# Kernel optimization log

Measured on AMD Instinct MI355X. Metric: run time of the kernel, lower is better.

Reference implementation:

```python
import jax, jax.numpy as jnp
import numpy as np

B, N, NFEAT, NHID, NOUT, NMLP, NCLASS = 32, 1024, 128, 64, 64, 128, 2
ALPHA = 0.2  # leaky relu slope
NEG = -9e15


def setup_inputs() -> dict:
    key = jax.random.key(0)
    ks = jax.random.split(key, 12)
    x = jax.random.normal(ks[0], (B, N, NFEAT), dtype=jnp.float32)
    x_mask = (jax.random.uniform(ks[1], (B, N)) < 0.9).astype(jnp.float32)
    adj = (jax.random.uniform(ks[2], (B, N, N)) < 0.05).astype(jnp.float32)
    adj = jnp.maximum(adj, jnp.eye(N, dtype=jnp.float32)[None])  # self loops
    s = 0.02
    W0 = jax.random.normal(ks[3], (NFEAT, NHID), dtype=jnp.float32) * s
    a0 = jax.random.normal(ks[4], (2 * NHID, 1), dtype=jnp.float32) * s
    Wout = jax.random.normal(ks[5], (NHID, NOUT), dtype=jnp.float32) * s
    aout = jax.random.normal(ks[6], (2 * NOUT, 1), dtype=jnp.float32) * s
    W1 = jax.random.normal(ks[7], (NOUT, NMLP), dtype=jnp.float32) * s
    b1 = jnp.zeros((NMLP,), dtype=jnp.float32)
    W2 = jax.random.normal(ks[8], (NMLP, NCLASS), dtype=jnp.float32) * s
    b2 = jnp.zeros((NCLASS,), dtype=jnp.float32)
    return {"x": x, "x_mask": x_mask, "adj": adj, "W0": W0, "a0": a0,
            "Wout": Wout, "aout": aout, "W1": W1, "b1": b1, "W2": W2, "b2": b2}


def _gat_layer(h, adj, W, a):
    # h: [B,N,F_in], W: [F_in,F_out], a: [2*F_out,1]
    Wh = jnp.einsum('bnf,fh->bnh', h, W)                 # [B,N,F_out]
    d = W.shape[1]
    f1 = Wh @ a[:d]                                      # [B,N,1]
    f2 = Wh @ a[d:]                                      # [B,N,1]
    e = jax.nn.leaky_relu(f1 + jnp.swapaxes(f2, 1, 2), ALPHA)  # [B,N,N]
    e = jnp.where(adj > 0, e, NEG)
    attn = jax.nn.softmax(e, axis=-1)
    return jnp.einsum('bnm,bmh->bnh', attn, Wh)


def reference(x, x_mask, adj, W0, a0, Wout, aout, W1, b1, W2, b2):
    # Only head 0 reaches out_att in the original (zip truncation); dropout is
    # identity in eval mode.
    h = jax.nn.elu(_gat_layer(x, adj, W0, a0))           # concat=True -> elu
    h = jax.nn.elu(_gat_layer(h, adj, Wout, aout))       # F.elu applied outside
    m = x_mask[..., None]
    g = jnp.sum(h * m, axis=1) / jnp.maximum(jnp.sum(x_mask, axis=1, keepdims=True), 1.0)  # masked mean readout [B,NOUT]
    return jax.nn.relu(g @ W1 + b1) @ W2 + b2            # [B,NCLASS]
```

## Files before the change

### kernel.cpp

```cpp
#include <hip/hip_runtime.h>
#include <math.h>

#define BB 32
#define NN 1024
#define NFEAT 128
#define ALPHA 0.2f
#define MAXD 128

#define WH1_TILE_BLOCKS (BB * NN / 64)
#define NBR_BLOCKS (BB * NN / 4)

template<int FIN>
__device__ __forceinline__ void wh_tile_body(
    const int blk, const int tid,
    const float* __restrict__ hin, const float* __restrict__ W,
    const float* __restrict__ a, float* __restrict__ Wh,
    float* __restrict__ f1, float* __restrict__ f2) {
  const int tx = tid & 15;
  const int ty = tid >> 4;
  const int row0 = blk * 64 + ty * 4;

  float4 acc[4];
#pragma unroll
  for (int i = 0; i < 4; ++i) acc[i] = make_float4(0.f, 0.f, 0.f, 0.f);

#pragma unroll 4
  for (int k = 0; k < FIN; k += 4) {
    float4 wv[4];
#pragma unroll
    for (int i = 0; i < 4; ++i)
      wv[i] = *reinterpret_cast<const float4*>(&W[(size_t)(k + i) * 64 + tx * 4]);
#pragma unroll
    for (int i = 0; i < 4; ++i) {
      const float4 xv = *reinterpret_cast<const float4*>(
          &hin[(size_t)(row0 + i) * FIN + k]);
      acc[i].x = fmaf(xv.x, wv[0].x, acc[i].x);
      acc[i].y = fmaf(xv.x, wv[0].y, acc[i].y);
      acc[i].z = fmaf(xv.x, wv[0].z, acc[i].z);
      acc[i].w = fmaf(xv.x, wv[0].w, acc[i].w);
      acc[i].x = fmaf(xv.y, wv[1].x, acc[i].x);
      acc[i].y = fmaf(xv.y, wv[1].y, acc[i].y);
      acc[i].z = fmaf(xv.y, wv[1].z, acc[i].z);
      acc[i].w = fmaf(xv.y, wv[1].w, acc[i].w);
      acc[i].x = fmaf(xv.z, wv[2].x, acc[i].x);
      acc[i].y = fmaf(xv.z, wv[2].y, acc[i].y);
      acc[i].z = fmaf(xv.z, wv[2].z, acc[i].z);
      acc[i].w = fmaf(xv.z, wv[2].w, acc[i].w);
      acc[i].x = fmaf(xv.w, wv[3].x, acc[i].x);
      acc[i].y = fmaf(xv.w, wv[3].y, acc[i].y);
      acc[i].z = fmaf(xv.w, wv[3].z, acc[i].z);
      acc[i].w = fmaf(xv.w, wv[3].w, acc[i].w);
    }
  }

  const float4 av1 = *reinterpret_cast<const float4*>(&a[tx * 4]);
  const float4 av2 = *reinterpret_cast<const float4*>(&a[64 + tx * 4]);
#pragma unroll
  for (int i = 0; i < 4; ++i) {
    const int row = row0 + i;
    *reinterpret_cast<float4*>(&Wh[(size_t)row * 64 + tx * 4]) = acc[i];
    float c1 = acc[i].x * av1.x + acc[i].y * av1.y + acc[i].z * av1.z + acc[i].w * av1.w;
    float c2 = acc[i].x * av2.x + acc[i].y * av2.y + acc[i].z * av2.z + acc[i].w * av2.w;
#pragma unroll
    for (int off = 8; off > 0; off >>= 1) {
      c1 += __shfl_xor(c1, off, 64);
      c2 += __shfl_xor(c2, off, 64);
    }
    if (tx == 0) { f1[row] = c1; f2[row] = c2; }
  }
}

__global__ __launch_bounds__(256) void wh1_nbr_kernel(
    const float* __restrict__ x, const float* __restrict__ W0,
    const float* __restrict__ a0, float* __restrict__ Wh,
    float* __restrict__ f1, float* __restrict__ f2,
    const float* __restrict__ adj, unsigned short* __restrict__ nbr,
    int* __restrict__ cnt) {
  if (blockIdx.x < WH1_TILE_BLOCKS) {
    wh_tile_body<NFEAT>(blockIdx.x, threadIdx.x, x, W0, a0, Wh, f1, f2);
    return;
  }
  const int row = (blockIdx.x - WH1_TILE_BLOCKS) * 4 + (threadIdx.x >> 6);
  const int lane = threadIdx.x & 63;
  const float* adjrow = adj + (size_t)row * NN;
  unsigned short* nrow = nbr + (size_t)row * MAXD;
  int count = 0;
#pragma unroll
  for (int c = 0; c < NN / 64; ++c) {
    const float av = adjrow[c * 64 + lane];
    const bool on = av > 0.f;
    const unsigned long long mask = __ballot(on);
    const int pos = __popcll(mask & ((1ull << lane) - 1ull));
    if (on && count + pos < MAXD)
      nrow[count + pos] = (unsigned short)(c * 64 + lane);
    count += __popcll(mask);
  }
  if (lane == 0) cnt[row] = count < MAXD ? count : MAXD;
}

template<bool FUSE>
__global__ __launch_bounds__(256) void attn_kernel(
    const unsigned short* __restrict__ nbr, const int* __restrict__ cnt,
    const float* __restrict__ f1, const float* __restrict__ f2,
    const float* __restrict__ Wh,
    const float* __restrict__ Wnext, const float* __restrict__ anext,
    float* __restrict__ WhOut, float* __restrict__ f1o,
    float* __restrict__ f2o, float* __restrict__ hOut) {
  __shared__ float ps[4][MAXD];
  __shared__ unsigned short msh[4][MAXD];
  __shared__ float h1s[4][64];
  const int wv = threadIdx.x >> 6, lane = threadIdx.x & 63;
  const int j = blockIdx.x;
  const int batch = (j & 7) + 8 * (j >> 11);
  const int chunk = (j >> 3) & 255;
  const int row = (batch * 256 + chunk) * 4 + wv;
  const int b = batch;

  int count = cnt[row];
  if (count > MAXD) count = MAXD;
  const unsigned short* nrow = nbr + (size_t)row * MAXD;
  const float* f2b = f2 + (size_t)b * NN;
  const float f1n = f1[row];

  int m0 = 0, m1 = 0;
  const bool on0 = lane < count, on1 = 64 + lane < count;
  float e0 = -3e38f, e1 = -3e38f;
  if (on0) { m0 = nrow[lane];      float v = f1n + f2b[m0]; e0 = v > 0.f ? v : ALPHA * v; }
  if (on1) { m1 = nrow[64 + lane]; float v = f1n + f2b[m1]; e1 = v > 0.f ? v : ALPHA * v; }
  float lmax = fmaxf(e0, e1);
#pragma unroll
  for (int off = 32; off > 0; off >>= 1) lmax = fmaxf(lmax, __shfl_xor(lmax, off, 64));
  float p0 = on0 ? __expf(e0 - lmax) : 0.f;
  float p1 = on1 ? __expf(e1 - lmax) : 0.f;
  float ls = p0 + p1;
#pragma unroll
  for (int off = 32; off > 0; off >>= 1) ls += __shfl_xor(ls, off, 64);
  const float inv = 1.f / ls;
  ps[wv][lane] = p0 * inv;  ps[wv][64 + lane] = p1 * inv;
  msh[wv][lane] = (unsigned short)m0;  msh[wv][64 + lane] = (unsigned short)m1;

  const float* Whb = Wh + (size_t)b * (NN * 64);
  float a0 = 0.f, a1 = 0.f, a2 = 0.f, a3 = 0.f;
  const int c4 = count & ~3;
  int k = 0;
  for (; k < c4; k += 4) {
    const float4  p4 = *reinterpret_cast<const float4*>(&ps[wv][k]);
    const ushort4 i4 = *reinterpret_cast<const ushort4*>(&msh[wv][k]);
    a0 = fmaf(p4.x, Whb[(size_t)i4.x * 64 + lane], a0);
    a1 = fmaf(p4.y, Whb[(size_t)i4.y * 64 + lane], a1);
    a2 = fmaf(p4.z, Whb[(size_t)i4.z * 64 + lane], a2);
    a3 = fmaf(p4.w, Whb[(size_t)i4.w * 64 + lane], a3);
  }
  for (; k < count; ++k)
    a0 = fmaf(ps[wv][k], Whb[(size_t)msh[wv][k] * 64 + lane], a0);
  const float acc = (a0 + a1) + (a2 + a3);
  const float hval = acc > 0.f ? acc : expm1f(acc);

  if (!FUSE) {
    hOut[(size_t)row * 64 + lane] = hval;
    return;
  }
  h1s[wv][lane] = hval;
  float s = 0.f;
#pragma unroll 8
  for (int f = 0; f < 64; ++f)
    s = fmaf(h1s[wv][f], Wnext[f * 64 + lane], s);
  WhOut[(size_t)row * 64 + lane] = s;
  float c1 = s * anext[lane];
  float c2 = s * anext[64 + lane];
#pragma unroll
  for (int off = 32; off > 0; off >>= 1) {
    c1 += __shfl_xor(c1, off, 64);
    c2 += __shfl_xor(c2, off, 64);
  }
  if (lane == 0) { f1o[row] = c1; f2o[row] = c2; }
}

__global__ __launch_bounds__(256) void readout_part_kernel(
    const float* __restrict__ h2, const float* __restrict__ mask,
    float* __restrict__ part, float* __restrict__ mspart) {
  const int blk = blockIdx.x;
  const int b = blk >> 4, c = blk & 15;
  const int tid = threadIdx.x;
  const int h = tid & 63, w = tid >> 6;
  __shared__ float agg[256];
  const float* mrow = mask + (size_t)b * NN + c * 64;
  const float* hb = h2 + ((size_t)b * NN + c * 64) * 64;

  float acc = 0.f;
#pragma unroll
  for (int i = 0; i < 16; ++i) {
    const int n = w * 16 + i;
    const float mv = mrow[n];
    if (mv != 0.f) acc += mv * hb[(size_t)n * 64 + h];
  }
  agg[tid] = acc;
  if (w == 1) {
    float ms = mrow[h];
#pragma unroll
    for (int off = 32; off > 0; off >>= 1) ms += __shfl_xor(ms, off, 64);
    if (h == 0) mspart[blk] = ms;
  }
  __syncthreads();
  if (w == 0)
    part[(size_t)blk * 64 + h] = agg[h] + agg[64 + h] + agg[128 + h] + agg[192 + h];
}

__global__ __launch_bounds__(128) void mlp_kernel(
    const float* __restrict__ part, const float* __restrict__ mspart,
    const float* __restrict__ W1, const float* __restrict__ b1,
    const float* __restrict__ W2, const float* __restrict__ b2,
    float* __restrict__ outp) {
  const int b = blockIdx.x;
  const int tid = threadIdx.x;
  __shared__ float g[64];
  __shared__ float hid[128];
  __shared__ float denom_s;

  if (tid == 64) {
    float s = 0.f;
#pragma unroll
    for (int c = 0; c < 16; ++c) s += mspart[b * 16 + c];
    denom_s = fmaxf(s, 1.0f);
  }
  float gsum = 0.f;
  if (tid < 64) {
#pragma unroll
    for (int c = 0; c < 16; ++c) gsum += part[((size_t)b * 16 + c) * 64 + tid];
  }
  __syncthreads();
  if (tid < 64) g[tid] = gsum / denom_s;
  __syncthreads();
  float s = b1[tid];
#pragma unroll 8
  for (int k = 0; k < 64; ++k) s += g[k] * W1[k * 128 + tid];
  hid[tid] = fmaxf(s, 0.f);
  __syncthreads();
  if (tid < 2) {
    float o = b2[tid];
    for (int j = 0; j < 128; ++j) o += hid[j] * W2[j * 2 + tid];
    outp[b * 2 + tid] = o;
  }
}

extern "C" void kernel_launch(void* const* d_in, const int* in_sizes, int n_in,
                              void* d_out, int out_size, void* d_ws, size_t ws_size,
                              hipStream_t stream) {
  const float* x      = (const float*)d_in[0];
  const float* x_mask = (const float*)d_in[1];
  const float* adj    = (const float*)d_in[2];
  const float* W0     = (const float*)d_in[3];
  const float* a0     = (const float*)d_in[4];
  const float* Wout   = (const float*)d_in[5];
  const float* aout   = (const float*)d_in[6];
  const float* W1     = (const float*)d_in[7];
  const float* b1     = (const float*)d_in[8];
  const float* W2     = (const float*)d_in[9];
  const float* b2     = (const float*)d_in[10];
  float* out = (float*)d_out;

  const int rows = BB * NN;

  float* ws = (float*)d_ws;
  float* Wh  = ws;
  float* Wh2 = Wh + (size_t)rows * 64;
  float* f1  = Wh2 + (size_t)rows * 64;
  float* f2  = f1 + rows;
  float* f1b = f2 + rows;
  float* f2b = f1b + rows;
  int*   cnt = (int*)(f2b + rows);
  unsigned short* nbr = (unsigned short*)(cnt + rows);
  float* part   = (float*)(nbr + (size_t)rows * MAXD);
  float* mspart = part + BB * 16 * 64;
  float* h2 = Wh;

  wh1_nbr_kernel<<<WH1_TILE_BLOCKS + NBR_BLOCKS, 256, 0, stream>>>(
      x, W0, a0, Wh, f1, f2, adj, nbr, cnt);
  attn_kernel<true><<<NBR_BLOCKS, 256, 0, stream>>>(
      nbr, cnt, f1, f2, Wh, Wout, aout, Wh2, f1b, f2b, nullptr);
  attn_kernel<false><<<NBR_BLOCKS, 256, 0, stream>>>(
      nbr, cnt, f1b, f2b, Wh2, nullptr, nullptr, nullptr, nullptr, nullptr, h2);
  readout_part_kernel<<<BB * 16, 256, 0, stream>>>(h2, x_mask, part, mspart);
  mlp_kernel<<<BB, 128, 0, stream>>>(part, mspart, W1, b1, W2, b2, out);
}
```

Measured before the change: 122.9 us.

## Split neighbor build into per-row kernel, fuse readout into layer-two attention

The adjacency scan now runs as its own kernel with one block per row. Each wave reads four floats per lane with a float4 load, compacts neighbors through four ballots, and merges them via shared memory. The second attention layer now applies the mask and reduces four rows into a partial sum, so the h2 write and the separate readout kernel go away. The MLP kernel reduces these 256 partials per batch. The gather loop is unrolled to eight accumulators for more memory-level parallelism. This adds a launch, since the Wh1 and neighbor-build stages are no longer co-scheduled, and the MLP kernel now does a larger reduction.

Result: faster. 119.3 us (-2.9%).

```diff
diff --git a/kernel.cpp b/kernel.cpp
--- a/kernel.cpp
+++ b/kernel.cpp
@@ -8,7 +8,7 @@
 #define MAXD 128
 
 #define WH1_TILE_BLOCKS (BB * NN / 64)
-#define NBR_BLOCKS (BB * NN / 4)
+#define ATTN_BLOCKS (BB * NN / 4)
 
 template<int FIN>
 __device__ __forceinline__ void wh_tile_body(
@@ -70,42 +70,115 @@
   }
 }
 
-__global__ __launch_bounds__(256) void wh1_nbr_kernel(
+__global__ __launch_bounds__(256) void wh1_kernel(
     const float* __restrict__ x, const float* __restrict__ W0,
     const float* __restrict__ a0, float* __restrict__ Wh,
-    float* __restrict__ f1, float* __restrict__ f2,
+    float* __restrict__ f1, float* __restrict__ f2) {
+  wh_tile_body<NFEAT>(blockIdx.x, threadIdx.x, x, W0, a0, Wh, f1, f2);
+}
+
+__global__ __launch_bounds__(256) void nbr_build_kernel(
     const float* __restrict__ adj, unsigned short* __restrict__ nbr,
     int* __restrict__ cnt) {
-  if (blockIdx.x < WH1_TILE_BLOCKS) {
-    wh_tile_body<NFEAT>(blockIdx.x, threadIdx.x, x, W0, a0, Wh, f1, f2);
-    return;
-  }
-  const int row = (blockIdx.x - WH1_TILE_BLOCKS) * 4 + (threadIdx.x >> 6);
-  const int lane = threadIdx.x & 63;
+  __shared__ unsigned short stageW[4][128];
+  __shared__ unsigned short merged[MAXD];
+  __shared__ int cnts[4];
+  const int row = blockIdx.x;
+  const int wv = threadIdx.x >> 6, lane = threadIdx.x & 63;
   const float* adjrow = adj + (size_t)row * NN;
-  unsigned short* nrow = nbr + (size_t)row * MAXD;
-  int count = 0;
-#pragma unroll
-  for (int c = 0; c < NN / 64; ++c) {
-    const float av = adjrow[c * 64 + lane];
-    const bool on = av > 0.f;
-    const unsigned long long mask = __ballot(on);
-    const int pos = __popcll(mask & ((1ull << lane) - 1ull));
-    if (on && count + pos < MAXD)
-      nrow[count + pos] = (unsigned short)(c * 64 + lane);
-    count += __popcll(mask);
-  }
-  if (lane == 0) cnt[row] = count < MAXD ? count : MAXD;
-}
-
-template<bool FUSE>
-__global__ __launch_bounds__(256) void attn_kernel(
+
+  const float4 av = *reinterpret_cast<const float4*>(&adjrow[wv * 256 + lane * 4]);
+  if (threadIdx.x < 64)
+    reinterpret_cast<unsigned int*>(merged)[threadIdx.x] = 0u;
+
+  const unsigned long long lmask = (1ull << lane) - 1ull;
+  const int m = (av.x > 0.f ? 1 : 0) | (av.y > 0.f ? 2 : 0) |
+                (av.z > 0.f ? 4 : 0) | (av.w > 0.f ? 8 : 0);
+  const unsigned long long b0 = __ballot(m & 1);
+  const unsigned long long b1 = __ballot(m & 2);
+  const unsigned long long b2 = __ballot(m & 4);
+  const unsigned long long b3 = __ballot(m & 8);
+  int base = __popcll(b0 & lmask) + __popcll(b1 & lmask) +
+             __popcll(b2 & lmask) + __popcll(b3 & lmask);
+  const int e0 = wv * 256 + lane * 4;
+  if (m & 1) { if (base < 128) stageW[wv][base] = (unsigned short)(e0);     ++base; }
+  if (m & 2) { if (base < 128) stageW[wv][base] = (unsigned short)(e0 + 1); ++base; }
+  if (m & 4) { if (base < 128) stageW[wv][base] = (unsigned short)(e0 + 2); ++base; }
+  if (m & 8) { if (base < 128) stageW[wv][base] = (unsigned short)(e0 + 3); ++base; }
+  if (lane == 0)
+    cnts[wv] = __popcll(b0) + __popcll(b1) + __popcll(b2) + __popcll(b3);
+  __syncthreads();
+  const int c0 = cnts[0], c1 = cnts[1], c2 = cnts[2], c3 = cnts[3];
+  const int off = (wv == 0) ? 0 : (wv == 1) ? c0 : (wv == 2) ? c0 + c1 : c0 + c1 + c2;
+  const int cw  = (wv == 0) ? c0 : (wv == 1) ? c1 : (wv == 2) ? c2 : c3;
+  if (lane < cw && off + lane < MAXD) merged[off + lane] = stageW[wv][lane];
+  if (64 + lane < cw && off + 64 + lane < MAXD)
+    merged[off + 64 + lane] = stageW[wv][64 + lane];
+  __syncthreads();
+  if (threadIdx.x < 64)
+    reinterpret_cast<unsigned int*>(nbr + (size_t)row * MAXD)[threadIdx.x] =
+        reinterpret_cast<const unsigned int*>(merged)[threadIdx.x];
+  if (threadIdx.x == 0) {
+    const int total = c0 + c1 + c2 + c3;
+    cnt[row] = total < MAXD ? total : MAXD;
+  }
+}
+
+__device__ __forceinline__ void attn_softmax(
+    const unsigned short* __restrict__ nrow, const int count,
+    const float f1n, const float* __restrict__ f2b,
+    float* ps, unsigned short* msh, const int lane) {
+  int m0 = 0, m1 = 0;
+  const bool on0 = lane < count, on1 = 64 + lane < count;
+  float e0 = -3e38f, e1 = -3e38f;
+  if (on0) { m0 = nrow[lane];      float v = f1n + f2b[m0]; e0 = v > 0.f ? v : ALPHA * v; }
+  if (on1) { m1 = nrow[64 + lane]; float v = f1n + f2b[m1]; e1 = v > 0.f ? v : ALPHA * v; }
+  float lmax = fmaxf(e0, e1);
+#pragma unroll
+  for (int off = 32; off > 0; off >>= 1) lmax = fmaxf(lmax, __shfl_xor(lmax, off, 64));
+  float p0 = on0 ? __expf(e0 - lmax) : 0.f;
+  float p1 = on1 ? __expf(e1 - lmax) : 0.f;
+  float ls = p0 + p1;
+#pragma unroll
+  for (int off = 32; off > 0; off >>= 1) ls += __shfl_xor(ls, off, 64);
+  const float inv = 1.f / ls;
+  ps[lane] = p0 * inv;  ps[64 + lane] = p1 * inv;
+  msh[lane] = (unsigned short)m0;  msh[64 + lane] = (unsigned short)m1;
+}
+
+__device__ __forceinline__ float attn_gather(
+    const float* ps, const unsigned short* msh, const int count,
+    const float* __restrict__ Whb, const int lane) {
+  float a0 = 0.f, a1 = 0.f, a2 = 0.f, a3 = 0.f;
+  float a4 = 0.f, a5 = 0.f, a6 = 0.f, a7 = 0.f;
+  const int c8 = count & ~7;
+  int k = 0;
+  for (; k < c8; k += 8) {
+    const float4  pa = *reinterpret_cast<const float4*>(&ps[k]);
+    const float4  pb = *reinterpret_cast<const float4*>(&ps[k + 4]);
+    const ushort4 ia = *reinterpret_cast<const ushort4*>(&msh[k]);
+    const ushort4 ib = *reinterpret_cast<const ushort4*>(&msh[k + 4]);
+    a0 = fmaf(pa.x, Whb[(size_t)ia.x * 64 + lane], a0);
+    a1 = fmaf(pa.y, Whb[(size_t)ia.y * 64 + lane], a1);
+    a2 = fmaf(pa.z, Whb[(size_t)ia.z * 64 + lane], a2);
+    a3 = fmaf(pa.w, Whb[(size_t)ia.w * 64 + lane], a3);
+    a4 = fmaf(pb.x, Whb[(size_t)ib.x * 64 + lane], a4);
+    a5 = fmaf(pb.y, Whb[(size_t)ib.y * 64 + lane], a5);
+    a6 = fmaf(pb.z, Whb[(size_t)ib.z * 64 + lane], a6);
+    a7 = fmaf(pb.w, Whb[(size_t)ib.w * 64 + lane], a7);
+  }
+  for (; k < count; ++k)
+    a0 = fmaf(ps[k], Whb[(size_t)msh[k] * 64 + lane], a0);
+  return ((a0 + a1) + (a2 + a3)) + ((a4 + a5) + (a6 + a7));
+}
+
+__global__ __launch_bounds__(256) void attn1_kernel(
     const unsigned short* __restrict__ nbr, const int* __restrict__ cnt,
     const float* __restrict__ f1, const float* __restrict__ f2,
     const float* __restrict__ Wh,
     const float* __restrict__ Wnext, const float* __restrict__ anext,
     float* __restrict__ WhOut, float* __restrict__ f1o,
-    float* __restrict__ f2o, float* __restrict__ hOut) {
+    float* __restrict__ f2o) {
   __shared__ float ps[4][MAXD];
   __shared__ unsigned short msh[4][MAXD];
   __shared__ float h1s[4][64];
@@ -114,52 +187,15 @@
   const int batch = (j & 7) + 8 * (j >> 11);
   const int chunk = (j >> 3) & 255;
   const int row = (batch * 256 + chunk) * 4 + wv;
-  const int b = batch;
 
   int count = cnt[row];
   if (count > MAXD) count = MAXD;
-  const unsigned short* nrow = nbr + (size_t)row * MAXD;
-  const float* f2b = f2 + (size_t)b * NN;
-  const float f1n = f1[row];
-
-  int m0 = 0, m1 = 0;
-  const bool on0 = lane < count, on1 = 64 + lane < count;
-  float e0 = -3e38f, e1 = -3e38f;
-  if (on0) { m0 = nrow[lane];      float v = f1n + f2b[m0]; e0 = v > 0.f ? v : ALPHA * v; }
-  if (on1) { m1 = nrow[64 + lane]; float v = f1n + f2b[m1]; e1 = v > 0.f ? v : ALPHA * v; }
-  float lmax = fmaxf(e0, e1);
-#pragma unroll
-  for (int off = 32; off > 0; off >>= 1) lmax = fmaxf(lmax, __shfl_xor(lmax, off, 64));
-  float p0 = on0 ? __expf(e0 - lmax) : 0.f;
-  float p1 = on1 ? __expf(e1 - lmax) : 0.f;
-  float ls = p0 + p1;
-#pragma unroll
-  for (int off = 32; off > 0; off >>= 1) ls += __shfl_xor(ls, off, 64);
-  const float inv = 1.f / ls;
-  ps[wv][lane] = p0 * inv;  ps[wv][64 + lane] = p1 * inv;
-  msh[wv][lane] = (unsigned short)m0;  msh[wv][64 + lane] = (unsigned short)m1;
-
-  const float* Whb = Wh + (size_t)b * (NN * 64);
-  float a0 = 0.f, a1 = 0.f, a2 = 0.f, a3 = 0.f;
-  const int c4 = count & ~3;
-  int k = 0;
-  for (; k < c4; k += 4) {
-    const float4  p4 = *reinterpret_cast<const float4*>(&ps[wv][k]);
-    const ushort4 i4 = *reinterpret_cast<const ushort4*>(&msh[wv][k]);
-    a0 = fmaf(p4.x, Whb[(size_t)i4.x * 64 + lane], a0);
-    a1 = fmaf(p4.y, Whb[(size_t)i4.y * 64 + lane], a1);
-    a2 = fmaf(p4.z, Whb[(size_t)i4.z * 64 + lane], a2);
-    a3 = fmaf(p4.w, Whb[(size_t)i4.w * 64 + lane], a3);
-  }
-  for (; k < count; ++k)
-    a0 = fmaf(ps[wv][k], Whb[(size_t)msh[wv][k] * 64 + lane], a0);
-  const float acc = (a0 + a1) + (a2 + a3);
+  attn_softmax(nbr + (size_t)row * MAXD, count, f1[row],
+               f2 + (size_t)batch * NN, ps[wv], msh[wv], lane);
+  const float acc = attn_gather(ps[wv], msh[wv], count,
+                                Wh + (size_t)batch * (NN * 64), lane);
   const float hval = acc > 0.f ? acc : expm1f(acc);
 
-  if (!FUSE) {
-    hOut[(size_t)row * 64 + lane] = hval;
-    return;
-  }
   h1s[wv][lane] = hval;
   float s = 0.f;
 #pragma unroll 8
@@ -176,69 +212,75 @@
   if (lane == 0) { f1o[row] = c1; f2o[row] = c2; }
 }
 
-__global__ __launch_bounds__(256) void readout_part_kernel(
-    const float* __restrict__ h2, const float* __restrict__ mask,
-    float* __restrict__ part, float* __restrict__ mspart) {
-  const int blk = blockIdx.x;
-  const int b = blk >> 4, c = blk & 15;
-  const int tid = threadIdx.x;
-  const int h = tid & 63, w = tid >> 6;
-  __shared__ float agg[256];
-  const float* mrow = mask + (size_t)b * NN + c * 64;
-  const float* hb = h2 + ((size_t)b * NN + c * 64) * 64;
-
-  float acc = 0.f;
-#pragma unroll
-  for (int i = 0; i < 16; ++i) {
-    const int n = w * 16 + i;
-    const float mv = mrow[n];
-    if (mv != 0.f) acc += mv * hb[(size_t)n * 64 + h];
-  }
-  agg[tid] = acc;
-  if (w == 1) {
-    float ms = mrow[h];
-#pragma unroll
-    for (int off = 32; off > 0; off >>= 1) ms += __shfl_xor(ms, off, 64);
-    if (h == 0) mspart[blk] = ms;
-  }
-  __syncthreads();
-  if (w == 0)
-    part[(size_t)blk * 64 + h] = agg[h] + agg[64 + h] + agg[128 + h] + agg[192 + h];
-}
-
-__global__ __launch_bounds__(128) void mlp_kernel(
-    const float* __restrict__ part, const float* __restrict__ mspart,
+__global__ __launch_bounds__(256) void attn2_kernel(
+    const unsigned short* __restrict__ nbr, const int* __restrict__ cnt,
+    const float* __restrict__ f1, const float* __restrict__ f2,
+    const float* __restrict__ Wh, const float* __restrict__ mask,
+    float* __restrict__ part2) {
+  __shared__ float ps[4][MAXD];
+  __shared__ unsigned short msh[4][MAXD];
+  __shared__ float agg[4][64];
+  const int wv = threadIdx.x >> 6, lane = threadIdx.x & 63;
+  const int j = blockIdx.x;
+  const int batch = (j & 7) + 8 * (j >> 11);
+  const int chunk = (j >> 3) & 255;
+  const int row = (batch * 256 + chunk) * 4 + wv;
+
+  int count = cnt[row];
+  if (count > MAXD) count = MAXD;
+  attn_softmax(nbr + (size_t)row * MAXD, count, f1[row],
+               f2 + (size_t)batch * NN, ps[wv], msh[wv], lane);
+  const float acc = attn_gather(ps[wv], msh[wv], count,
+                                Wh + (size_t)batch * (NN * 64), lane);
+  const float hval = acc > 0.f ? acc : expm1f(acc);
+
+  const float mv = mask[row];
+  agg[wv][lane] = mv * hval;
+  __syncthreads();
+  if (wv == 0)
+    part2[(size_t)(batch * 256 + chunk) * 64 + lane] =
+        (agg[0][lane] + agg[1][lane]) + (agg[2][lane] + agg[3][lane]);
+}
+
+__global__ __launch_bounds__(256) void mlp2_kernel(
+    const float* __restrict__ part2, const float* __restrict__ mask,
     const float* __restrict__ W1, const float* __restrict__ b1,
     const float* __restrict__ W2, const float* __restrict__ b2,
     float* __restrict__ outp) {
   const int b = blockIdx.x;
   const int tid = threadIdx.x;
+  const int wv = tid >> 6, lane = tid & 63;
+  __shared__ float aggG[4][64];
+  __shared__ float msW[4];
   __shared__ float g[64];
   __shared__ float hid[128];
-  __shared__ float denom_s;
-
-  if (tid == 64) {
-    float s = 0.f;
-#pragma unroll
-    for (int c = 0; c < 16; ++c) s += mspart[b * 16 + c];
-    denom_s = fmaxf(s, 1.0f);
-  }
-  float gsum = 0.f;
-  if (tid < 64) {
-#pragma unroll
-    for (int c = 0; c < 16; ++c) gsum += part[((size_t)b * 16 + c) * 64 + tid];
-  }
-  __syncthreads();
-  if (tid < 64) g[tid] = gsum / denom_s;
-  __syncthreads();
-  float s = b1[tid];
+
+  const float4 mv4 = *reinterpret_cast<const float4*>(&mask[(size_t)b * NN + tid * 4]);
+  float ms = (mv4.x + mv4.y) + (mv4.z + mv4.w);
+#pragma unroll
+  for (int off = 32; off > 0; off >>= 1) ms += __shfl_xor(ms, off, 64);
+  if (lane == 0) msW[wv] = ms;
+
+  float gs = 0.f;
+  const float* pb = part2 + ((size_t)b * 256 + wv * 64) * 64 + lane;
 #pragma unroll 8
-  for (int k = 0; k < 64; ++k) s += g[k] * W1[k * 128 + tid];
-  hid[tid] = fmaxf(s, 0.f);
+  for (int i = 0; i < 64; ++i) gs += pb[(size_t)i * 64];
+  aggG[wv][lane] = gs;
+  __syncthreads();
+  const float denom = fmaxf((msW[0] + msW[1]) + (msW[2] + msW[3]), 1.0f);
+  if (tid < 64)
+    g[tid] = ((aggG[0][tid] + aggG[1][tid]) + (aggG[2][tid] + aggG[3][tid])) / denom;
+  __syncthreads();
+  if (tid < 128) {
+    float s = b1[tid];
+#pragma unroll 8
+    for (int k = 0; k < 64; ++k) s += g[k] * W1[k * 128 + tid];
+    hid[tid] = fmaxf(s, 0.f);
+  }
   __syncthreads();
   if (tid < 2) {
     float o = b2[tid];
-    for (int j = 0; j < 128; ++j) o += hid[j] * W2[j * 2 + tid];
+    for (int jj = 0; jj < 128; ++jj) o += hid[jj] * W2[jj * 2 + tid];
     outp[b * 2 + tid] = o;
   }
 }
@@ -270,16 +312,13 @@
   float* f2b = f1b + rows;
   int*   cnt = (int*)(f2b + rows);
   unsigned short* nbr = (unsigned short*)(cnt + rows);
-  float* part   = (float*)(nbr + (size_t)rows * MAXD);
-  float* mspart = part + BB * 16 * 64;
-  float* h2 = Wh;
-
-  wh1_nbr_kernel<<<WH1_TILE_BLOCKS + NBR_BLOCKS, 256, 0, stream>>>(
-      x, W0, a0, Wh, f1, f2, adj, nbr, cnt);
-  attn_kernel<true><<<NBR_BLOCKS, 256, 0, stream>>>(
-      nbr, cnt, f1, f2, Wh, Wout, aout, Wh2, f1b, f2b, nullptr);
-  attn_kernel<false><<<NBR_BLOCKS, 256, 0, stream>>>(
-      nbr, cnt, f1b, f2b, Wh2, nullptr, nullptr, nullptr, nullptr, nullptr, h2);
-  readout_part_kernel<<<BB * 16, 256, 0, stream>>>(h2, x_mask, part, mspart);
-  mlp_kernel<<<BB, 128, 0, stream>>>(part, mspart, W1, b1, W2, b2, out);
-}
+  float* part2 = (float*)(nbr + (size_t)rows * MAXD);
+
+  nbr_build_kernel<<<rows, 256, 0, stream>>>(adj, nbr, cnt);
+  wh1_kernel<<<WH1_TILE_BLOCKS, 256, 0, stream>>>(x, W0, a0, Wh, f1, f2);
+  attn1_kernel<<<ATTN_BLOCKS, 256, 0, stream>>>(
+      nbr, cnt, f1, f2, Wh, Wout, aout, Wh2, f1b, f2b);
+  attn2_kernel<<<ATTN_BLOCKS, 256, 0, stream>>>(
+      nbr, cnt, f1b, f2b, Wh2, x_mask, part2);
+  mlp2_kernel<<<BB, 256, 0, stream>>>(part2, x_mask, W1, b1, W2, b2, out);
+}
```
